# Kernel tuning notes

Hardware: AMD Instinct MI355X
Metric: run time of the kernel (lower is better)

The kernel has to match this reference:

```python
import jax, jax.numpy as jnp
import numpy as np

BINS = 256

def setup_inputs() -> dict:
    key = jax.random.key(0)
    x = jax.random.normal(key, (64, 3, 512, 512), dtype=jnp.float32)
    return {"x": x}

def reference(x):
    bins = BINS

    def equalize_one(img):
        # img: (C, H, W) -- flattened wholesale, matching the torch per-index loop
        flat = img.reshape(-1)
        mn = flat.min()
        mx = flat.max()
        norm = (flat - mn) * (bins - 1) / (mx - mn + 1e-8)
        norm = jnp.clip(norm, 0, bins - 1)
        idx = norm.astype(jnp.int32)  # bucket index per pixel
        hist = jnp.zeros((bins,), jnp.float32).at[idx].add(1.0)  # bincount
        cdf = jnp.cumsum(hist)
        cdf_norm = (cdf - cdf.min()) / (cdf.max() - cdf.min() + 1e-8)
        return cdf_norm[idx].reshape(img.shape)  # gather equalized values

    return jax.vmap(equalize_one)(x)
```

## Files before the change

### kernel.cpp

```cpp
#include <hip/hip_runtime.h>

#define NUM_BINS 256
#define NPI (3*512*512)
#define TPB 256
#define MM_BLOCKS 16
#define NSUB 32
#define SUBSTRIDE 257
#define G_VEC 8

__device__ __forceinline__ int bin_of(float v, float mn, float denom) {
  float norm = (v - mn) * 255.0f / denom;
  norm = fminf(fmaxf(norm, 0.0f), 255.0f);
  return (int)norm;
}

__device__ __forceinline__ unsigned pack4(int b0, int b1, int b2, int b3) {
  return (unsigned)b0 | ((unsigned)b1 << 8) | ((unsigned)b2 << 16) | ((unsigned)b3 << 24);
}

__global__ void minmax_k(const float4* __restrict__ x,
                         float* __restrict__ mmn, float* __restrict__ mmx) {
  const int chunk4 = NPI / 4 / MM_BLOCKS;
  int img = blockIdx.x / MM_BLOCKS;
  int blk = blockIdx.x % MM_BLOCKS;
  const float4* p = x + (size_t)img * (NPI/4) + (size_t)blk * chunk4;
  float mn = 3.4e38f, mx = -3.4e38f;
  for (int i = threadIdx.x; i < chunk4; i += TPB) {
    float4 v = p[i];
    mn = fminf(mn, fminf(fminf(v.x, v.y), fminf(v.z, v.w)));
    mx = fmaxf(mx, fmaxf(fmaxf(v.x, v.y), fmaxf(v.z, v.w)));
  }
  for (int off = 32; off > 0; off >>= 1) {
    mn = fminf(mn, __shfl_down(mn, off));
    mx = fmaxf(mx, __shfl_down(mx, off));
  }
  __shared__ float smn[4], smx[4];
  int wave = threadIdx.x >> 6, lane = threadIdx.x & 63;
  if (lane == 0) { smn[wave] = mn; smx[wave] = mx; }
  __syncthreads();
  if (threadIdx.x == 0) {
    mmn[blockIdx.x] = fminf(fminf(smn[0], smn[1]), fminf(smn[2], smn[3]));
    mmx[blockIdx.x] = fmaxf(fmaxf(smx[0], smx[1]), fmaxf(smx[2], smx[3]));
  }
}

__global__ void hist_k(const float4* __restrict__ x,
                       const float* __restrict__ mmn, const float* __restrict__ mmx,
                       int* __restrict__ histblk, unsigned* __restrict__ bins32) {
  __shared__ int sh[NSUB * SUBSTRIDE];
  __shared__ float s_mn, s_dn;
  for (int i = threadIdx.x; i < NSUB * SUBSTRIDE; i += TPB) sh[i] = 0;
  const int chunk4 = NPI / 4 / MM_BLOCKS;
  int img = blockIdx.x / MM_BLOCKS;
  int blk = blockIdx.x % MM_BLOCKS;
  if (threadIdx.x < MM_BLOCKS) {
    float a = mmn[img * MM_BLOCKS + threadIdx.x];
    float b = mmx[img * MM_BLOCKS + threadIdx.x];
    for (int off = 8; off > 0; off >>= 1) {
      a = fminf(a, __shfl_down(a, off));
      b = fmaxf(b, __shfl_down(b, off));
    }
    if (threadIdx.x == 0) { s_mn = a; s_dn = b - a + 1e-8f; }
  }
  __syncthreads();
  float mn = s_mn, denom = s_dn;
  size_t gbase = (size_t)img * (NPI/4) + (size_t)blk * chunk4;
  const float4* p = x + gbase;
  int* mysub = sh + (threadIdx.x & (NSUB - 1)) * SUBSTRIDE;
  bool wb = (bins32 != nullptr);
  for (int i = threadIdx.x; i < chunk4; i += TPB * 4) {
    float4 v0 = p[i];
    float4 v1 = p[i + TPB];
    float4 v2 = p[i + 2*TPB];
    float4 v3 = p[i + 3*TPB];
    int b00 = bin_of(v0.x, mn, denom), b01 = bin_of(v0.y, mn, denom);
    int b02 = bin_of(v0.z, mn, denom), b03 = bin_of(v0.w, mn, denom);
    int b10 = bin_of(v1.x, mn, denom), b11 = bin_of(v1.y, mn, denom);
    int b12 = bin_of(v1.z, mn, denom), b13 = bin_of(v1.w, mn, denom);
    int b20 = bin_of(v2.x, mn, denom), b21 = bin_of(v2.y, mn, denom);
    int b22 = bin_of(v2.z, mn, denom), b23 = bin_of(v2.w, mn, denom);
    int b30 = bin_of(v3.x, mn, denom), b31 = bin_of(v3.y, mn, denom);
    int b32 = bin_of(v3.z, mn, denom), b33 = bin_of(v3.w, mn, denom);
    atomicAdd(&mysub[b00], 1); atomicAdd(&mysub[b01], 1);
    atomicAdd(&mysub[b02], 1); atomicAdd(&mysub[b03], 1);
    atomicAdd(&mysub[b10], 1); atomicAdd(&mysub[b11], 1);
    atomicAdd(&mysub[b12], 1); atomicAdd(&mysub[b13], 1);
    atomicAdd(&mysub[b20], 1); atomicAdd(&mysub[b21], 1);
    atomicAdd(&mysub[b22], 1); atomicAdd(&mysub[b23], 1);
    atomicAdd(&mysub[b30], 1); atomicAdd(&mysub[b31], 1);
    atomicAdd(&mysub[b32], 1); atomicAdd(&mysub[b33], 1);
    if (wb) {
      bins32[gbase + i]           = pack4(b00, b01, b02, b03);
      bins32[gbase + i + TPB]     = pack4(b10, b11, b12, b13);
      bins32[gbase + i + 2*TPB]   = pack4(b20, b21, b22, b23);
      bins32[gbase + i + 3*TPB]   = pack4(b30, b31, b32, b33);
    }
  }
  __syncthreads();
  int bin = threadIdx.x;
  int s = 0;
  #pragma unroll
  for (int c = 0; c < NSUB; ++c) s += sh[c * SUBSTRIDE + bin];
  histblk[blockIdx.x * NUM_BINS + bin] = s;
}

__global__ void scan_k(const int* __restrict__ histblk, float* __restrict__ cdfn) {
  __shared__ int s[NUM_BINS];
  int img = blockIdx.x, t = threadIdx.x;
  int v = 0;
  #pragma unroll
  for (int b = 0; b < MM_BLOCKS; ++b)
    v += histblk[(img * MM_BLOCKS + b) * NUM_BINS + t];
  s[t] = v;
  __syncthreads();
  for (int off = 1; off < NUM_BINS; off <<= 1) {
    int add = (t >= off) ? s[t - off] : 0;
    __syncthreads();
    s[t] += add;
    __syncthreads();
  }
  int cdf = s[t], c0 = s[0], cN = s[NUM_BINS - 1];
  cdfn[img * NUM_BINS + t] = (float)(cdf - c0) / ((float)(cN - c0) + 1e-8f);
}

__global__ void gather_bins_k(const unsigned* __restrict__ bins32,
                              const float* __restrict__ cdfn,
                              float4* __restrict__ out) {
  __shared__ float c[NUM_BINS];
  const int f4pi = NPI / 4;
  const int CHUNK = TPB * G_VEC;
  const int bpi = f4pi / CHUNK;
  int img = blockIdx.x / bpi;
  int blk = blockIdx.x % bpi;
  c[threadIdx.x] = cdfn[img * NUM_BINS + threadIdx.x];
  __syncthreads();
  size_t base = (size_t)img * f4pi + (size_t)blk * CHUNK + threadIdx.x;
  unsigned bv[G_VEC];
  #pragma unroll
  for (int j = 0; j < G_VEC; ++j) bv[j] = bins32[base + (size_t)j * TPB];
  #pragma unroll
  for (int j = 0; j < G_VEC; ++j) {
    unsigned b = bv[j];
    float4 o;
    o.x = c[b & 255u];
    o.y = c[(b >> 8) & 255u];
    o.z = c[(b >> 16) & 255u];
    o.w = c[b >> 24];
    out[base + (size_t)j * TPB] = o;
  }
}

__global__ void gather_x_k(const float4* __restrict__ x,
                           const float* __restrict__ mmn, const float* __restrict__ mmx,
                           const float* __restrict__ cdfn,
                           float4* __restrict__ out) {
  __shared__ float c[NUM_BINS];
  __shared__ float s_mn, s_dn;
  const int f4pi = NPI / 4;
  const int CHUNK = TPB * 4;
  const int bpi = f4pi / CHUNK;
  int img = blockIdx.x / bpi;
  int blk = blockIdx.x % bpi;
  c[threadIdx.x] = cdfn[img * NUM_BINS + threadIdx.x];
  if (threadIdx.x < MM_BLOCKS) {
    float a = mmn[img * MM_BLOCKS + threadIdx.x];
    float b = mmx[img * MM_BLOCKS + threadIdx.x];
    for (int off = 8; off > 0; off >>= 1) {
      a = fminf(a, __shfl_down(a, off));
      b = fmaxf(b, __shfl_down(b, off));
    }
    if (threadIdx.x == 0) { s_mn = a; s_dn = b - a + 1e-8f; }
  }
  __syncthreads();
  float mn = s_mn, denom = s_dn;
  size_t base = (size_t)img * f4pi + (size_t)blk * CHUNK + threadIdx.x;
  #pragma unroll
  for (int j = 0; j < 4; ++j) {
    float4 v = x[base + (size_t)j * TPB];
    float4 o;
    o.x = c[bin_of(v.x, mn, denom)];
    o.y = c[bin_of(v.y, mn, denom)];
    o.z = c[bin_of(v.z, mn, denom)];
    o.w = c[bin_of(v.w, mn, denom)];
    out[base + (size_t)j * TPB] = o;
  }
}

extern "C" void kernel_launch(void* const* d_in, const int* in_sizes, int n_in,
                              void* d_out, int out_size, void* d_ws, size_t ws_size,
                              hipStream_t stream) {
  const float* x = (const float*)d_in[0];
  float* out = (float*)d_out;
  int B = in_sizes[0] / NPI;

  char* ws = (char*)d_ws;
  float* mmn = (float*)ws;
  float* mmx = mmn + (size_t)B * MM_BLOCKS;
  int* histblk = (int*)(mmx + (size_t)B * MM_BLOCKS);
  float* cdfn = (float*)(histblk + (size_t)B * MM_BLOCKS * NUM_BINS);
  unsigned* bins32 = (unsigned*)(cdfn + (size_t)B * NUM_BINS);
  size_t need = (size_t)((char*)bins32 - ws) + (size_t)B * NPI;
  bool use_bins = (ws_size >= need);

  minmax_k<<<B * MM_BLOCKS, TPB, 0, stream>>>((const float4*)x, mmn, mmx);
  hist_k<<<B * MM_BLOCKS, TPB, 0, stream>>>((const float4*)x, mmn, mmx, histblk,
                                            use_bins ? bins32 : nullptr);
  scan_k<<<B, NUM_BINS, 0, stream>>>(histblk, cdfn);
  if (use_bins) {
    gather_bins_k<<<B * (NPI/4/(TPB*G_VEC)), TPB, 0, stream>>>(bins32, cdfn, (float4*)out);
  } else {
    gather_x_k<<<B * (NPI/4/(TPB*4)), TPB, 0, stream>>>((const float4*)x, mmn, mmx, cdfn,
                                                        (float4*)out);
  }
}
```

Baseline: 392.9 us.

## Fuse histogram equalization stages into one cooperative persistent kernel

Combines minmax, histogram, scan and gather into a single cooperative kernel separated by grid-wide syncs, launched with an occupancy-limited grid and falling back to the multi-kernel path on failure. The gather stage now uses nontemporal stores for the output. The aim is to remove launch gaps and inter-kernel drain. In exchange it adds grid.sync overhead and reduces gather parallelism to one block per histogram chunk with a serial loop.

```diff
diff --git a/kernel.cpp b/kernel.cpp
--- a/kernel.cpp
+++ b/kernel.cpp
@@ -1,4 +1,7 @@
 #include <hip/hip_runtime.h>
+#include <hip/hip_cooperative_groups.h>
+
+namespace cg = cooperative_groups;
 
 #define NUM_BINS 256
 #define NPI (3*512*512)
@@ -8,6 +11,8 @@
 #define SUBSTRIDE 257
 #define G_VEC 8
 
+typedef float f32x4 __attribute__((ext_vector_type(4)));
+
 __device__ __forceinline__ int bin_of(float v, float mn, float denom) {
   float norm = (v - mn) * 255.0f / denom;
   norm = fminf(fmaxf(norm, 0.0f), 255.0f);
@@ -16,6 +21,171 @@
 
 __device__ __forceinline__ unsigned pack4(int b0, int b1, int b2, int b3) {
   return (unsigned)b0 | ((unsigned)b1 << 8) | ((unsigned)b2 << 16) | ((unsigned)b3 << 24);
+}
+
+__global__ void __launch_bounds__(TPB, 4)
+fused_k(const float4* __restrict__ x, int B,
+        float* __restrict__ mmn, float* __restrict__ mmx,
+        int* __restrict__ histblk, float* __restrict__ cdfn,
+        unsigned* __restrict__ bins32, float4* __restrict__ out,
+        int use_bins) {
+  cg::grid_group grid = cg::this_grid();
+  __shared__ int sh[NSUB * SUBSTRIDE];
+  __shared__ float smn[4], smx[4];
+  __shared__ float s_mn, s_dn;
+  const int nvb = B * MM_BLOCKS;
+  const int chunk4 = NPI / 4 / MM_BLOCKS;
+
+  for (int vb = blockIdx.x; vb < nvb; vb += gridDim.x) {
+    int img = vb / MM_BLOCKS, blk = vb % MM_BLOCKS;
+    const float4* p = x + (size_t)img * (NPI/4) + (size_t)blk * chunk4;
+    float mn = 3.4e38f, mx = -3.4e38f;
+    for (int i = threadIdx.x; i < chunk4; i += TPB) {
+      float4 v = p[i];
+      mn = fminf(mn, fminf(fminf(v.x, v.y), fminf(v.z, v.w)));
+      mx = fmaxf(mx, fmaxf(fmaxf(v.x, v.y), fmaxf(v.z, v.w)));
+    }
+    for (int off = 32; off > 0; off >>= 1) {
+      mn = fminf(mn, __shfl_down(mn, off));
+      mx = fmaxf(mx, __shfl_down(mx, off));
+    }
+    int wave = threadIdx.x >> 6, lane = threadIdx.x & 63;
+    if (lane == 0) { smn[wave] = mn; smx[wave] = mx; }
+    __syncthreads();
+    if (threadIdx.x == 0) {
+      mmn[vb] = fminf(fminf(smn[0], smn[1]), fminf(smn[2], smn[3]));
+      mmx[vb] = fmaxf(fmaxf(smx[0], smx[1]), fmaxf(smx[2], smx[3]));
+    }
+    __syncthreads();
+  }
+  grid.sync();
+
+  for (int vb = blockIdx.x; vb < nvb; vb += gridDim.x) {
+    int img = vb / MM_BLOCKS, blk = vb % MM_BLOCKS;
+    if (threadIdx.x < MM_BLOCKS) {
+      float a = mmn[img * MM_BLOCKS + threadIdx.x];
+      float b = mmx[img * MM_BLOCKS + threadIdx.x];
+      for (int off = 8; off > 0; off >>= 1) {
+        a = fminf(a, __shfl_down(a, off));
+        b = fmaxf(b, __shfl_down(b, off));
+      }
+      if (threadIdx.x == 0) { s_mn = a; s_dn = b - a + 1e-8f; }
+    }
+    for (int i = threadIdx.x; i < NSUB * SUBSTRIDE; i += TPB) sh[i] = 0;
+    __syncthreads();
+    float mn = s_mn, denom = s_dn;
+    size_t gbase = (size_t)img * (NPI/4) + (size_t)blk * chunk4;
+    const float4* p = x + gbase;
+    int* mysub = sh + (threadIdx.x & (NSUB - 1)) * SUBSTRIDE;
+    for (int i = threadIdx.x; i < chunk4; i += TPB * 4) {
+      float4 v0 = p[i];
+      float4 v1 = p[i + TPB];
+      float4 v2 = p[i + 2*TPB];
+      float4 v3 = p[i + 3*TPB];
+      int b00 = bin_of(v0.x, mn, denom), b01 = bin_of(v0.y, mn, denom);
+      int b02 = bin_of(v0.z, mn, denom), b03 = bin_of(v0.w, mn, denom);
+      int b10 = bin_of(v1.x, mn, denom), b11 = bin_of(v1.y, mn, denom);
+      int b12 = bin_of(v1.z, mn, denom), b13 = bin_of(v1.w, mn, denom);
+      int b20 = bin_of(v2.x, mn, denom), b21 = bin_of(v2.y, mn, denom);
+      int b22 = bin_of(v2.z, mn, denom), b23 = bin_of(v2.w, mn, denom);
+      int b30 = bin_of(v3.x, mn, denom), b31 = bin_of(v3.y, mn, denom);
+      int b32 = bin_of(v3.z, mn, denom), b33 = bin_of(v3.w, mn, denom);
+      atomicAdd(&mysub[b00], 1); atomicAdd(&mysub[b01], 1);
+      atomicAdd(&mysub[b02], 1); atomicAdd(&mysub[b03], 1);
+      atomicAdd(&mysub[b10], 1); atomicAdd(&mysub[b11], 1);
+      atomicAdd(&mysub[b12], 1); atomicAdd(&mysub[b13], 1);
+      atomicAdd(&mysub[b20], 1); atomicAdd(&mysub[b21], 1);
+      atomicAdd(&mysub[b22], 1); atomicAdd(&mysub[b23], 1);
+      atomicAdd(&mysub[b30], 1); atomicAdd(&mysub[b31], 1);
+      atomicAdd(&mysub[b32], 1); atomicAdd(&mysub[b33], 1);
+      if (use_bins) {
+        bins32[gbase + i]         = pack4(b00, b01, b02, b03);
+        bins32[gbase + i + TPB]   = pack4(b10, b11, b12, b13);
+        bins32[gbase + i + 2*TPB] = pack4(b20, b21, b22, b23);
+        bins32[gbase + i + 3*TPB] = pack4(b30, b31, b32, b33);
+      }
+    }
+    __syncthreads();
+    int bin = threadIdx.x;
+    int s = 0;
+    #pragma unroll
+    for (int c2 = 0; c2 < NSUB; ++c2) s += sh[c2 * SUBSTRIDE + bin];
+    histblk[vb * NUM_BINS + bin] = s;
+    __syncthreads();
+  }
+  grid.sync();
+
+  for (int img = blockIdx.x; img < B; img += gridDim.x) {
+    int t = threadIdx.x;
+    int v = 0;
+    #pragma unroll
+    for (int b = 0; b < MM_BLOCKS; ++b)
+      v += histblk[(img * MM_BLOCKS + b) * NUM_BINS + t];
+    sh[t] = v;
+    __syncthreads();
+    for (int off = 1; off < NUM_BINS; off <<= 1) {
+      int add = (t >= off) ? sh[t - off] : 0;
+      __syncthreads();
+      sh[t] += add;
+      __syncthreads();
+    }
+    int cdf = sh[t], c0 = sh[0], cN = sh[NUM_BINS - 1];
+    cdfn[img * NUM_BINS + t] = (float)(cdf - c0) / ((float)(cN - c0) + 1e-8f);
+    __syncthreads();
+  }
+  grid.sync();
+
+  float* cf = (float*)sh;
+  const int f4pi = NPI / 4;
+  for (int vb = blockIdx.x; vb < nvb; vb += gridDim.x) {
+    int img = vb / MM_BLOCKS, blk = vb % MM_BLOCKS;
+    cf[threadIdx.x] = cdfn[img * NUM_BINS + threadIdx.x];
+    if (!use_bins && threadIdx.x < MM_BLOCKS) {
+      float a = mmn[img * MM_BLOCKS + threadIdx.x];
+      float b = mmx[img * MM_BLOCKS + threadIdx.x];
+      for (int off = 8; off > 0; off >>= 1) {
+        a = fminf(a, __shfl_down(a, off));
+        b = fmaxf(b, __shfl_down(b, off));
+      }
+      if (threadIdx.x == 0) { s_mn = a; s_dn = b - a + 1e-8f; }
+    }
+    __syncthreads();
+    size_t base = (size_t)img * f4pi + (size_t)blk * chunk4 + threadIdx.x;
+    if (use_bins) {
+      for (int it = 0; it < chunk4 / (TPB * G_VEC); ++it) {
+        size_t b0 = base + (size_t)it * TPB * G_VEC;
+        unsigned bv[G_VEC];
+        #pragma unroll
+        for (int j = 0; j < G_VEC; ++j) bv[j] = bins32[b0 + (size_t)j * TPB];
+        #pragma unroll
+        for (int j = 0; j < G_VEC; ++j) {
+          unsigned b = bv[j];
+          f32x4 o;
+          o.x = cf[b & 255u];
+          o.y = cf[(b >> 8) & 255u];
+          o.z = cf[(b >> 16) & 255u];
+          o.w = cf[b >> 24];
+          __builtin_nontemporal_store(o, (f32x4*)&out[b0 + (size_t)j * TPB]);
+        }
+      }
+    } else {
+      float mn = s_mn, denom = s_dn;
+      for (int it = 0; it < chunk4 / (TPB * 4); ++it) {
+        size_t b0 = base + (size_t)it * TPB * 4;
+        #pragma unroll
+        for (int j = 0; j < 4; ++j) {
+          float4 v = x[b0 + (size_t)j * TPB];
+          f32x4 o;
+          o.x = cf[bin_of(v.x, mn, denom)];
+          o.y = cf[bin_of(v.y, mn, denom)];
+          o.z = cf[bin_of(v.z, mn, denom)];
+          o.w = cf[bin_of(v.w, mn, denom)];
+          __builtin_nontemporal_store(o, (f32x4*)&out[b0 + (size_t)j * TPB]);
+        }
+      }
+    }
+    __syncthreads();
+  }
 }
 
 __global__ void minmax_k(const float4* __restrict__ x,
@@ -90,10 +260,10 @@
     atomicAdd(&mysub[b30], 1); atomicAdd(&mysub[b31], 1);
     atomicAdd(&mysub[b32], 1); atomicAdd(&mysub[b33], 1);
     if (wb) {
-      bins32[gbase + i]           = pack4(b00, b01, b02, b03);
-      bins32[gbase + i + TPB]     = pack4(b10, b11, b12, b13);
-      bins32[gbase + i + 2*TPB]   = pack4(b20, b21, b22, b23);
-      bins32[gbase + i + 3*TPB]   = pack4(b30, b31, b32, b33);
+      bins32[gbase + i]         = pack4(b00, b01, b02, b03);
+      bins32[gbase + i + TPB]   = pack4(b10, b11, b12, b13);
+      bins32[gbase + i + 2*TPB] = pack4(b20, b21, b22, b23);
+      bins32[gbase + i + 3*TPB] = pack4(b30, b31, b32, b33);
     }
   }
   __syncthreads();
@@ -200,16 +370,41 @@
   float* cdfn = (float*)(histblk + (size_t)B * MM_BLOCKS * NUM_BINS);
   unsigned* bins32 = (unsigned*)(cdfn + (size_t)B * NUM_BINS);
   size_t need = (size_t)((char*)bins32 - ws) + (size_t)B * NPI;
-  bool use_bins = (ws_size >= need);
-
-  minmax_k<<<B * MM_BLOCKS, TPB, 0, stream>>>((const float4*)x, mmn, mmx);
-  hist_k<<<B * MM_BLOCKS, TPB, 0, stream>>>((const float4*)x, mmn, mmx, histblk,
-                                            use_bins ? bins32 : nullptr);
-  scan_k<<<B, NUM_BINS, 0, stream>>>(histblk, cdfn);
-  if (use_bins) {
-    gather_bins_k<<<B * (NPI/4/(TPB*G_VEC)), TPB, 0, stream>>>(bins32, cdfn, (float4*)out);
-  } else {
-    gather_x_k<<<B * (NPI/4/(TPB*4)), TPB, 0, stream>>>((const float4*)x, mmn, mmx, cdfn,
-                                                        (float4*)out);
-  }
-}
+  int use_bins = (ws_size >= need) ? 1 : 0;
+
+  static int max_blocks = -1;
+  if (max_blocks < 0) {
+    int per_cu = 0;
+    if (hipOccupancyMaxActiveBlocksPerMultiprocessor(&per_cu, fused_k, TPB, 0)
+            != hipSuccess || per_cu < 1)
+      per_cu = 1;
+    int ncu = 256;
+    hipDeviceProp_t prop;
+    if (hipGetDeviceProperties(&prop, 0) == hipSuccess && prop.multiProcessorCount > 0)
+      ncu = prop.multiProcessorCount;
+    max_blocks = per_cu * ncu;
+  }
+  int nvb = B * MM_BLOCKS;
+  int grid = (nvb < max_blocks) ? nvb : max_blocks;
+
+  const float4* x4 = (const float4*)x;
+  float4* out4 = (float4*)out;
+  unsigned* binsp = use_bins ? bins32 : nullptr;
+  void* kargs[] = { (void*)&x4, (void*)&B, (void*)&mmn, (void*)&mmx,
+                    (void*)&histblk, (void*)&cdfn, (void*)&binsp, (void*)&out4,
+                    (void*)&use_bins };
+  hipError_t err = hipLaunchCooperativeKernel(fused_k, dim3(grid), dim3(TPB),
+                                              kargs, 0, stream);
+  if (err != hipSuccess) {
+    minmax_k<<<B * MM_BLOCKS, TPB, 0, stream>>>((const float4*)x, mmn, mmx);
+    hist_k<<<B * MM_BLOCKS, TPB, 0, stream>>>((const float4*)x, mmn, mmx, histblk,
+                                              use_bins ? bins32 : nullptr);
+    scan_k<<<B, NUM_BINS, 0, stream>>>(histblk, cdfn);
+    if (use_bins) {
+      gather_bins_k<<<B * (NPI/4/(TPB*G_VEC)), TPB, 0, stream>>>(bins32, cdfn, (float4*)out);
+    } else {
+      gather_x_k<<<B * (NPI/4/(TPB*4)), TPB, 0, stream>>>((const float4*)x, mmn, mmx, cdfn,
+                                                          (float4*)out);
+    }
+  }
+}
```

After: 649.8 us. 65.4% more time.

## Fuse CDF scan into gather kernel, add nontemporal stores, widen minmax grid

Applied to the files above, without the earlier changes.

The scan kernel is folded into the gather kernel on the bins path. Each gather block recomputes the per-image CDF from the block histograms and then walks a larger chunk of packed bins, writing the output with nontemporal stores. The minmax pass now uses 32 blocks per image with unrolling, and the histogram loop processes 8 float4s per iteration. This removes a kernel launch and its serialization, at the cost of redundant scan work in every gather block and more register pressure in the histogram kernel.

```diff
diff --git a/kernel.cpp b/kernel.cpp
--- a/kernel.cpp
+++ b/kernel.cpp
@@ -3,10 +3,14 @@
 #define NUM_BINS 256
 #define NPI (3*512*512)
 #define TPB 256
+#define MMX_BLOCKS 32
 #define MM_BLOCKS 16
+#define GB_PER_IMG 32
 #define NSUB 32
 #define SUBSTRIDE 257
 #define G_VEC 8
+
+typedef float f32x4 __attribute__((ext_vector_type(4)));
 
 __device__ __forceinline__ int bin_of(float v, float mn, float denom) {
   float norm = (v - mn) * 255.0f / denom;
@@ -20,11 +24,12 @@
 
 __global__ void minmax_k(const float4* __restrict__ x,
                          float* __restrict__ mmn, float* __restrict__ mmx) {
-  const int chunk4 = NPI / 4 / MM_BLOCKS;
-  int img = blockIdx.x / MM_BLOCKS;
-  int blk = blockIdx.x % MM_BLOCKS;
+  const int chunk4 = NPI / 4 / MMX_BLOCKS;
+  int img = blockIdx.x / MMX_BLOCKS;
+  int blk = blockIdx.x % MMX_BLOCKS;
   const float4* p = x + (size_t)img * (NPI/4) + (size_t)blk * chunk4;
   float mn = 3.4e38f, mx = -3.4e38f;
+  #pragma unroll 4
   for (int i = threadIdx.x; i < chunk4; i += TPB) {
     float4 v = p[i];
     mn = fminf(mn, fminf(fminf(v.x, v.y), fminf(v.z, v.w)));
@@ -41,6 +46,20 @@
   if (threadIdx.x == 0) {
     mmn[blockIdx.x] = fminf(fminf(smn[0], smn[1]), fminf(smn[2], smn[3]));
     mmx[blockIdx.x] = fmaxf(fmaxf(smx[0], smx[1]), fmaxf(smx[2], smx[3]));
+  }
+}
+
+__device__ __forceinline__ void load_minmax(const float* __restrict__ mmn,
+                                            const float* __restrict__ mmx,
+                                            int img, float* s_mn, float* s_dn) {
+  if (threadIdx.x < MMX_BLOCKS) {
+    float a = mmn[img * MMX_BLOCKS + threadIdx.x];
+    float b = mmx[img * MMX_BLOCKS + threadIdx.x];
+    for (int off = MMX_BLOCKS / 2; off > 0; off >>= 1) {
+      a = fminf(a, __shfl_down(a, off));
+      b = fmaxf(b, __shfl_down(b, off));
+    }
+    if (threadIdx.x == 0) { *s_mn = a; *s_dn = b - a + 1e-8f; }
   }
 }
 
@@ -49,51 +68,40 @@
                        int* __restrict__ histblk, unsigned* __restrict__ bins32) {
   __shared__ int sh[NSUB * SUBSTRIDE];
   __shared__ float s_mn, s_dn;
+  load_minmax(mmn, mmx, blockIdx.x / MM_BLOCKS, &s_mn, &s_dn);
   for (int i = threadIdx.x; i < NSUB * SUBSTRIDE; i += TPB) sh[i] = 0;
   const int chunk4 = NPI / 4 / MM_BLOCKS;
   int img = blockIdx.x / MM_BLOCKS;
   int blk = blockIdx.x % MM_BLOCKS;
-  if (threadIdx.x < MM_BLOCKS) {
-    float a = mmn[img * MM_BLOCKS + threadIdx.x];
-    float b = mmx[img * MM_BLOCKS + threadIdx.x];
-    for (int off = 8; off > 0; off >>= 1) {
-      a = fminf(a, __shfl_down(a, off));
-      b = fmaxf(b, __shfl_down(b, off));
-    }
-    if (threadIdx.x == 0) { s_mn = a; s_dn = b - a + 1e-8f; }
-  }
   __syncthreads();
   float mn = s_mn, denom = s_dn;
   size_t gbase = (size_t)img * (NPI/4) + (size_t)blk * chunk4;
   const float4* p = x + gbase;
   int* mysub = sh + (threadIdx.x & (NSUB - 1)) * SUBSTRIDE;
   bool wb = (bins32 != nullptr);
-  for (int i = threadIdx.x; i < chunk4; i += TPB * 4) {
-    float4 v0 = p[i];
-    float4 v1 = p[i + TPB];
-    float4 v2 = p[i + 2*TPB];
-    float4 v3 = p[i + 3*TPB];
-    int b00 = bin_of(v0.x, mn, denom), b01 = bin_of(v0.y, mn, denom);
-    int b02 = bin_of(v0.z, mn, denom), b03 = bin_of(v0.w, mn, denom);
-    int b10 = bin_of(v1.x, mn, denom), b11 = bin_of(v1.y, mn, denom);
-    int b12 = bin_of(v1.z, mn, denom), b13 = bin_of(v1.w, mn, denom);
-    int b20 = bin_of(v2.x, mn, denom), b21 = bin_of(v2.y, mn, denom);
-    int b22 = bin_of(v2.z, mn, denom), b23 = bin_of(v2.w, mn, denom);
-    int b30 = bin_of(v3.x, mn, denom), b31 = bin_of(v3.y, mn, denom);
-    int b32 = bin_of(v3.z, mn, denom), b33 = bin_of(v3.w, mn, denom);
-    atomicAdd(&mysub[b00], 1); atomicAdd(&mysub[b01], 1);
-    atomicAdd(&mysub[b02], 1); atomicAdd(&mysub[b03], 1);
-    atomicAdd(&mysub[b10], 1); atomicAdd(&mysub[b11], 1);
-    atomicAdd(&mysub[b12], 1); atomicAdd(&mysub[b13], 1);
-    atomicAdd(&mysub[b20], 1); atomicAdd(&mysub[b21], 1);
-    atomicAdd(&mysub[b22], 1); atomicAdd(&mysub[b23], 1);
-    atomicAdd(&mysub[b30], 1); atomicAdd(&mysub[b31], 1);
-    atomicAdd(&mysub[b32], 1); atomicAdd(&mysub[b33], 1);
+  for (int i = threadIdx.x; i < chunk4; i += TPB * 8) {
+    float4 v[8];
+    #pragma unroll
+    for (int k = 0; k < 8; ++k) v[k] = p[i + k * TPB];
+    int b[8][4];
+    #pragma unroll
+    for (int k = 0; k < 8; ++k) {
+      b[k][0] = bin_of(v[k].x, mn, denom);
+      b[k][1] = bin_of(v[k].y, mn, denom);
+      b[k][2] = bin_of(v[k].z, mn, denom);
+      b[k][3] = bin_of(v[k].w, mn, denom);
+    }
+    #pragma unroll
+    for (int k = 0; k < 8; ++k) {
+      atomicAdd(&mysub[b[k][0]], 1);
+      atomicAdd(&mysub[b[k][1]], 1);
+      atomicAdd(&mysub[b[k][2]], 1);
+      atomicAdd(&mysub[b[k][3]], 1);
+    }
     if (wb) {
-      bins32[gbase + i]           = pack4(b00, b01, b02, b03);
-      bins32[gbase + i + TPB]     = pack4(b10, b11, b12, b13);
-      bins32[gbase + i + 2*TPB]   = pack4(b20, b21, b22, b23);
-      bins32[gbase + i + 3*TPB]   = pack4(b30, b31, b32, b33);
+      #pragma unroll
+      for (int k = 0; k < 8; ++k)
+        bins32[gbase + i + k * TPB] = pack4(b[k][0], b[k][1], b[k][2], b[k][3]);
     }
   }
   __syncthreads();
@@ -102,6 +110,53 @@
   #pragma unroll
   for (int c = 0; c < NSUB; ++c) s += sh[c * SUBSTRIDE + bin];
   histblk[blockIdx.x * NUM_BINS + bin] = s;
+}
+
+__global__ void gather_bins_k(const unsigned* __restrict__ bins32,
+                              const int* __restrict__ histblk,
+                              float4* __restrict__ out) {
+  __shared__ int s[NUM_BINS];
+  __shared__ float c[NUM_BINS];
+  const int f4pi = NPI / 4;
+  const int chunk4 = f4pi / GB_PER_IMG;
+  const int ITERS = chunk4 / (TPB * G_VEC);
+  int img = blockIdx.x / GB_PER_IMG;
+  int blk = blockIdx.x % GB_PER_IMG;
+  int t = threadIdx.x;
+  int v = 0;
+  #pragma unroll
+  for (int b = 0; b < MM_BLOCKS; ++b)
+    v += histblk[(img * MM_BLOCKS + b) * NUM_BINS + t];
+  s[t] = v;
+  __syncthreads();
+  for (int off = 1; off < NUM_BINS; off <<= 1) {
+    int add = (t >= off) ? s[t - off] : 0;
+    __syncthreads();
+    s[t] += add;
+    __syncthreads();
+  }
+  {
+    int cdf = s[t], c0 = s[0], cN = s[NUM_BINS - 1];
+    c[t] = (float)(cdf - c0) / ((float)(cN - c0) + 1e-8f);
+  }
+  __syncthreads();
+  size_t base = (size_t)img * f4pi + (size_t)blk * chunk4 + threadIdx.x;
+  for (int it = 0; it < ITERS; ++it) {
+    size_t b0 = base + (size_t)it * TPB * G_VEC;
+    unsigned bv[G_VEC];
+    #pragma unroll
+    for (int j = 0; j < G_VEC; ++j) bv[j] = bins32[b0 + (size_t)j * TPB];
+    #pragma unroll
+    for (int j = 0; j < G_VEC; ++j) {
+      unsigned b = bv[j];
+      f32x4 o;
+      o.x = c[b & 255u];
+      o.y = c[(b >> 8) & 255u];
+      o.z = c[(b >> 16) & 255u];
+      o.w = c[b >> 24];
+      __builtin_nontemporal_store(o, (f32x4*)&out[b0 + (size_t)j * TPB]);
+    }
+  }
 }
 
 __global__ void scan_k(const int* __restrict__ histblk, float* __restrict__ cdfn) {
@@ -121,33 +176,6 @@
   }
   int cdf = s[t], c0 = s[0], cN = s[NUM_BINS - 1];
   cdfn[img * NUM_BINS + t] = (float)(cdf - c0) / ((float)(cN - c0) + 1e-8f);
-}
-
-__global__ void gather_bins_k(const unsigned* __restrict__ bins32,
-                              const float* __restrict__ cdfn,
-                              float4* __restrict__ out) {
-  __shared__ float c[NUM_BINS];
-  const int f4pi = NPI / 4;
-  const int CHUNK = TPB * G_VEC;
-  const int bpi = f4pi / CHUNK;
-  int img = blockIdx.x / bpi;
-  int blk = blockIdx.x % bpi;
-  c[threadIdx.x] = cdfn[img * NUM_BINS + threadIdx.x];
-  __syncthreads();
-  size_t base = (size_t)img * f4pi + (size_t)blk * CHUNK + threadIdx.x;
-  unsigned bv[G_VEC];
-  #pragma unroll
-  for (int j = 0; j < G_VEC; ++j) bv[j] = bins32[base + (size_t)j * TPB];
-  #pragma unroll
-  for (int j = 0; j < G_VEC; ++j) {
-    unsigned b = bv[j];
-    float4 o;
-    o.x = c[b & 255u];
-    o.y = c[(b >> 8) & 255u];
-    o.z = c[(b >> 16) & 255u];
-    o.w = c[b >> 24];
-    out[base + (size_t)j * TPB] = o;
-  }
 }
 
 __global__ void gather_x_k(const float4* __restrict__ x,
@@ -162,27 +190,19 @@
   int img = blockIdx.x / bpi;
   int blk = blockIdx.x % bpi;
   c[threadIdx.x] = cdfn[img * NUM_BINS + threadIdx.x];
-  if (threadIdx.x < MM_BLOCKS) {
-    float a = mmn[img * MM_BLOCKS + threadIdx.x];
-    float b = mmx[img * MM_BLOCKS + threadIdx.x];
-    for (int off = 8; off > 0; off >>= 1) {
-      a = fminf(a, __shfl_down(a, off));
-      b = fmaxf(b, __shfl_down(b, off));
-    }
-    if (threadIdx.x == 0) { s_mn = a; s_dn = b - a + 1e-8f; }
-  }
+  load_minmax(mmn, mmx, img, &s_mn, &s_dn);
   __syncthreads();
   float mn = s_mn, denom = s_dn;
   size_t base = (size_t)img * f4pi + (size_t)blk * CHUNK + threadIdx.x;
   #pragma unroll
   for (int j = 0; j < 4; ++j) {
     float4 v = x[base + (size_t)j * TPB];
-    float4 o;
+    f32x4 o;
     o.x = c[bin_of(v.x, mn, denom)];
     o.y = c[bin_of(v.y, mn, denom)];
     o.z = c[bin_of(v.z, mn, denom)];
     o.w = c[bin_of(v.w, mn, denom)];
-    out[base + (size_t)j * TPB] = o;
+    __builtin_nontemporal_store(o, (f32x4*)&out[base + (size_t)j * TPB]);
   }
 }
 
@@ -195,20 +215,20 @@
 
   char* ws = (char*)d_ws;
   float* mmn = (float*)ws;
-  float* mmx = mmn + (size_t)B * MM_BLOCKS;
-  int* histblk = (int*)(mmx + (size_t)B * MM_BLOCKS);
+  float* mmx = mmn + (size_t)B * MMX_BLOCKS;
+  int* histblk = (int*)(mmx + (size_t)B * MMX_BLOCKS);
   float* cdfn = (float*)(histblk + (size_t)B * MM_BLOCKS * NUM_BINS);
   unsigned* bins32 = (unsigned*)(cdfn + (size_t)B * NUM_BINS);
   size_t need = (size_t)((char*)bins32 - ws) + (size_t)B * NPI;
   bool use_bins = (ws_size >= need);
 
-  minmax_k<<<B * MM_BLOCKS, TPB, 0, stream>>>((const float4*)x, mmn, mmx);
+  minmax_k<<<B * MMX_BLOCKS, TPB, 0, stream>>>((const float4*)x, mmn, mmx);
   hist_k<<<B * MM_BLOCKS, TPB, 0, stream>>>((const float4*)x, mmn, mmx, histblk,
                                             use_bins ? bins32 : nullptr);
-  scan_k<<<B, NUM_BINS, 0, stream>>>(histblk, cdfn);
   if (use_bins) {
-    gather_bins_k<<<B * (NPI/4/(TPB*G_VEC)), TPB, 0, stream>>>(bins32, cdfn, (float4*)out);
+    gather_bins_k<<<B * GB_PER_IMG, TPB, 0, stream>>>(bins32, histblk, (float4*)out);
   } else {
+    scan_k<<<B, NUM_BINS, 0, stream>>>(histblk, cdfn);
     gather_x_k<<<B * (NPI/4/(TPB*4)), TPB, 0, stream>>>((const float4*)x, mmn, mmx, cdfn,
                                                         (float4*)out);
   }
```

Measured after the change: 376.0 us. 1.04x faster.
